# Optimization experiments

Measured on AMD Instinct MI355X. Metric: run time of the kernel, lower is better.

The kernel has to match this reference:

```python
import jax, jax.numpy as jnp
import numpy as np

N_NODES = 100000
N_EDGES = 3200000
NEG_SLOPE = 0.2  # PyG GATConv default


def setup_inputs() -> dict:
    key = jax.random.key(0)
    ks = jax.random.split(key, 10)
    x = jax.random.normal(ks[0], (N_NODES, 2), dtype=jnp.float32)
    src = jax.random.randint(ks[1], (N_EDGES,), 0, N_NODES)
    dst = jax.random.randint(ks[2], (N_EDGES,), 0, N_NODES)
    edge_index = jnp.stack([src, dst]).astype(jnp.int64)
    edge_attr = jax.random.normal(ks[3], (N_EDGES, 4), dtype=jnp.float32)
    # layer 1: in=2, heads=4, out_per_head=8
    W1 = jax.random.normal(ks[4], (2, 32), dtype=jnp.float32) * 0.5
    att_src1 = jax.random.normal(ks[5], (4, 8), dtype=jnp.float32) * 0.3
    att_dst1 = jax.random.normal(ks[6], (4, 8), dtype=jnp.float32) * 0.3
    b1 = jnp.zeros((32,), dtype=jnp.float32)
    # layer 2: in=32, heads=1, out_per_head=2
    W2 = jax.random.normal(ks[7], (32, 2), dtype=jnp.float32) * 0.2
    att_src2 = jax.random.normal(ks[8], (1, 2), dtype=jnp.float32) * 0.3
    att_dst2 = jax.random.normal(ks[9], (1, 2), dtype=jnp.float32) * 0.3
    b2 = jnp.zeros((2,), dtype=jnp.float32)
    return {"x": x, "edge_index": edge_index, "edge_attr": edge_attr,
            "W1": W1, "att_src1": att_src1, "att_dst1": att_dst1, "b1": b1,
            "W2": W2, "att_src2": att_src2, "att_dst2": att_dst2, "b2": b2}


def _gat_conv(x, W, att_src, att_dst, bias, src, dst, heads, out_ch, concat, n):
    h = (x @ W).reshape(n, heads, out_ch)            # [N,H,C]
    a_s = (h * att_src).sum(-1)                       # [N,H]
    a_d = (h * att_dst).sum(-1)                       # [N,H]
    e = jax.nn.leaky_relu(a_s[src] + a_d[dst], NEG_SLOPE)  # [E,H]
    m = jax.ops.segment_max(e, dst, num_segments=n)   # stable softmax over dst groups
    ee = jnp.exp(e - m[dst])
    s = jax.ops.segment_sum(ee, dst, num_segments=n)
    alpha = ee / (s[dst] + 1e-16)                     # [E,H]
    out = jax.ops.segment_sum(h[src] * alpha[:, :, None], dst, num_segments=n)  # [N,H,C]
    out = out.reshape(n, heads * out_ch) if concat else out.mean(axis=1)
    return out + bias, alpha


def reference(x, edge_index, edge_attr, W1, att_src1, att_dst1, b1,
              W2, att_src2, att_dst2, b2):
    # edge_attr is accepted but ignored: GATConv was built without edge_dim.
    n = x.shape[0]
    loop = jnp.arange(n, dtype=edge_index.dtype)      # add_self_loops=True (PyG default)
    src = jnp.concatenate([edge_index[0], loop])
    dst = jnp.concatenate([edge_index[1], loop])
    h, alpha1 = _gat_conv(x, W1, att_src1, att_dst1, b1, src, dst, 4, 8, True, n)
    h = jax.nn.elu(h)
    out, alpha2 = _gat_conv(h, W2, att_src2, att_dst2, b2, src, dst, 1, 2, False, n)
    return out, alpha1, alpha2
```

## Files before the change

### kernel.cpp

```cpp
#include <hip/hip_runtime.h>
#include <hip/hip_fp16.h>
#include <math.h>

#define NEG_SLOPE 0.2f
#define BW 512
#define BSH 9
#define CAP 18432
#define NB_MAX 256

typedef float f4v __attribute__((ext_vector_type(4)));

__device__ __forceinline__ float lrelu(float v) {
    return v > 0.0f ? v : NEG_SLOPE * v;
}
__device__ __forceinline__ float pack2h(float a, float b) {
    __half2 h = __floats2half2_rn(a, b);
    return *reinterpret_cast<float*>(&h);
}
__device__ __forceinline__ float2 unpack2h(float f) {
    __half2 h = *reinterpret_cast<__half2*>(&f);
    return __half22float2(h);
}
__device__ __forceinline__ void nt_store4(float4 v, float4* p) {
    f4v x = {v.x, v.y, v.z, v.w};
    __builtin_nontemporal_store(x, (f4v*)p);
}

__global__ __launch_bounds__(256) void k_l1_node(
    const float* __restrict__ x, const float* __restrict__ W1,
    const float* __restrict__ asw, const float* __restrict__ adw,
    float4* __restrict__ ga, float2* __restrict__ as1h,
    float2* __restrict__ dpack2, int n)
{
    int i = blockIdx.x * blockDim.x + threadIdx.x;
    if (i >= n) return;
    float2 xv = ((const float2*)x)[i];
    float as[4] = {0.f, 0.f, 0.f, 0.f};
    float ad[4] = {0.f, 0.f, 0.f, 0.f};
    #pragma unroll
    for (int j = 0; j < 32; ++j) {
        float h = xv.x * W1[j] + xv.y * W1[32 + j];
        as[j >> 3] += h * asw[j];
        ad[j >> 3] += h * adw[j];
    }
    float p01 = pack2h(as[0], as[1]), p23 = pack2h(as[2], as[3]);
    ga[i] = make_float4(p01, p23, xv.x, xv.y);
    as1h[i] = make_float2(p01, p23);
    dpack2[2 * i] = make_float2(pack2h(ad[0], ad[1]), pack2h(ad[2], ad[3]));
}

__global__ __launch_bounds__(256) void k_init(int* __restrict__ bucketCursor, int nb)
{
    int t = blockIdx.x * blockDim.x + threadIdx.x;
    if (t < nb) bucketCursor[t] = 0;
}

__global__ __launch_bounds__(256) void k_binA(
    const int* __restrict__ ei, int* __restrict__ bucketCursor,
    unsigned int* __restrict__ binned, int E, int Et, int nb)
{
    __shared__ int cnt[NB_MAX], lscan[NB_MAX + 1], base[NB_MAX], lcur[NB_MAX];
    __shared__ unsigned int staging[4096];
    int t = threadIdx.x;
    int c0 = blockIdx.x * 4096;
    unsigned int ent[16];
    short bb[16];
    #pragma unroll
    for (int k = 0; k < 16; ++k) {
        int e = c0 + k * 256 + t;
        int s, d;
        if (e < E) {
            s = __builtin_nontemporal_load(&ei[e]);
            d = __builtin_nontemporal_load(&ei[E + e]);
        } else { s = e - E; d = s; }
        bool valid = e < Et;
        bb[k] = valid ? (short)(d >> BSH) : (short)(-1);
        ent[k] = ((unsigned int)s << BSH) | (unsigned int)(d & (BW - 1));
    }
    if (t < nb) cnt[t] = 0;
    __syncthreads();
    #pragma unroll
    for (int k = 0; k < 16; ++k)
        if (bb[k] >= 0) atomicAdd(&cnt[bb[k]], 1);
    __syncthreads();
    if (t == 0) {
        int r = 0;
        for (int b = 0; b < nb; ++b) { lscan[b] = r; r += cnt[b]; }
        lscan[nb] = r;
    }
    __syncthreads();
    if (t < nb) {
        if (cnt[t] > 0) base[t] = atomicAdd(&bucketCursor[t], cnt[t]);
        lcur[t] = lscan[t];
    }
    __syncthreads();
    #pragma unroll
    for (int k = 0; k < 16; ++k)
        if (bb[k] >= 0) {
            int p = atomicAdd(&lcur[bb[k]], 1);
            staging[p] = ent[k];
        }
    __syncthreads();
    int total = lscan[nb];
    for (int j = t; j < total; j += 256) {
        int lo = 0, hi = nb - 1;
        while (lo < hi) {
            int mid = (lo + hi + 1) >> 1;
            if (lscan[mid] <= j) lo = mid; else hi = mid - 1;
        }
        __builtin_nontemporal_store(staging[j],
            &binned[(size_t)lo * CAP + base[lo] + (j - lscan[lo])]);
    }
}

__global__ __launch_bounds__(1024) void k_binB(
    const unsigned int* __restrict__ binned, const int* __restrict__ bucketCursor,
    int* __restrict__ sorted, int2* __restrict__ rowrange, int n, int nb)
{
    __shared__ int cnt[BW], cur[BW];
    int t = threadIdx.x;
    int b = blockIdx.x;
    int m = bucketCursor[b];
    size_t base = (size_t)b * CAP;
    int node0 = b << BSH;
    if (t < BW) cnt[t] = 0;
    __syncthreads();
    for (int i = t; i < m; i += 1024)
        atomicAdd(&cnt[binned[base + i] & (BW - 1)], 1);
    __syncthreads();
    int deg = (t < BW) ? cnt[t] : 0;
    for (int off = 1; off < BW; off <<= 1) {
        int v = (t >= off && t < BW) ? cnt[t - off] : 0;
        __syncthreads();
        if (t < BW) cnt[t] += v;
        __syncthreads();
    }
    if (t < BW) {
        int ex = cnt[t] - deg;
        cur[t] = ex;
        int node = node0 + t;
        if (node < n)
            rowrange[node] = make_int2((int)base + ex, (int)base + ex + deg);
    }
    __syncthreads();
    for (int i = t; i < m; i += 1024) {
        unsigned int en = binned[base + i];
        int dl = (int)(en & (BW - 1));
        int p = atomicAdd(&cur[dl], 1);
        sorted[base + p] = (int)(en >> BSH);
    }
}

__global__ __launch_bounds__(128) void k_l1_gather(
    const int2* __restrict__ rowrange, const int* __restrict__ sorted,
    const float4* __restrict__ ga, float2* __restrict__ dpack2,
    const float* __restrict__ W1, const float* __restrict__ b1,
    const float* __restrict__ W2,
    const float* __restrict__ asw2, const float* __restrict__ adw2,
    float4* __restrict__ pk2f, float* __restrict__ a2s,
    float2* __restrict__ d2, int n)
{
    int d = blockIdx.x * blockDim.x + threadIdx.x;
    if (d >= n) return;
    int2 rr = rowrange[d];
    int beg = rr.x, end = rr.y;
    float2 adp = dpack2[2 * d];
    float2 ad01 = unpack2h(adp.x), ad23 = unpack2h(adp.y);
    float see[4] = {0.f, 0.f, 0.f, 0.f};
    float sx0[4] = {0.f, 0.f, 0.f, 0.f};
    float sx1[4] = {0.f, 0.f, 0.f, 0.f};
    int i = beg;
    for (; i + 4 <= end; i += 4) {
        int s0 = sorted[i], s1 = sorted[i + 1], s2 = sorted[i + 2], s3 = sorted[i + 3];
        float4 v0 = ga[s0], v1 = ga[s1], v2 = ga[s2], v3 = ga[s3];
        #pragma unroll
        for (int k = 0; k < 4; ++k) {
            float4 v = (k == 0) ? v0 : (k == 1) ? v1 : (k == 2) ? v2 : v3;
            float2 a01 = unpack2h(v.x), a23 = unpack2h(v.y);
            float e0 = __expf(lrelu(a01.x + ad01.x));
            float e1 = __expf(lrelu(a01.y + ad01.y));
            float e2 = __expf(lrelu(a23.x + ad23.x));
            float e3 = __expf(lrelu(a23.y + ad23.y));
            see[0] += e0; sx0[0] += e0 * v.z; sx1[0] += e0 * v.w;
            see[1] += e1; sx0[1] += e1 * v.z; sx1[1] += e1 * v.w;
            see[2] += e2; sx0[2] += e2 * v.z; sx1[2] += e2 * v.w;
            see[3] += e3; sx0[3] += e3 * v.z; sx1[3] += e3 * v.w;
        }
    }
    for (; i < end; ++i) {
        float4 v = ga[sorted[i]];
        float2 a01 = unpack2h(v.x), a23 = unpack2h(v.y);
        float e0 = __expf(lrelu(a01.x + ad01.x));
        float e1 = __expf(lrelu(a01.y + ad01.y));
        float e2 = __expf(lrelu(a23.x + ad23.x));
        float e3 = __expf(lrelu(a23.y + ad23.y));
        see[0] += e0; sx0[0] += e0 * v.z; sx1[0] += e0 * v.w;
        see[1] += e1; sx0[1] += e1 * v.z; sx1[1] += e1 * v.w;
        see[2] += e2; sx0[2] += e2 * v.z; sx1[2] += e2 * v.w;
        see[3] += e3; sx0[3] += e3 * v.z; sx1[3] += e3 * v.w;
    }
    float rs[4];
    #pragma unroll
    for (int h = 0; h < 4; ++h) rs[h] = 1.0f / (see[h] + 1e-16f);
    dpack2[2 * d + 1] = make_float2(pack2h(rs[0], rs[1]), pack2h(rs[2], rs[3]));
    float h20 = 0.f, h21 = 0.f;
    #pragma unroll
    for (int j = 0; j < 32; ++j) {
        int h = j >> 3;
        float num = W1[j] * sx0[h] + W1[32 + j] * sx1[h];
        float o = num * rs[h] + b1[j];
        float he = o > 0.f ? o : expm1f(o);
        h20 += he * W2[2 * j];
        h21 += he * W2[2 * j + 1];
    }
    float as2 = h20 * asw2[0] + h21 * asw2[1];
    float ad2 = h20 * adw2[0] + h21 * adw2[1];
    pk2f[d] = make_float4(as2, h20, h21, ad2);
    a2s[d] = as2;
    d2[d] = make_float2(ad2, 0.f);
}

__global__ __launch_bounds__(128) void k_l2_gather(
    const int2* __restrict__ rowrange, const int* __restrict__ sorted,
    const float4* __restrict__ pk2f, const float* __restrict__ b2,
    float2* __restrict__ d2, float* __restrict__ out, int n)
{
    int d = blockIdx.x * blockDim.x + threadIdx.x;
    if (d >= n) return;
    int2 rr = rowrange[d];
    int beg = rr.x, end = rr.y;
    float ad2 = d2[d].x;
    float se = 0.f, a0 = 0.f, a1 = 0.f;
    int i = beg;
    for (; i + 4 <= end; i += 4) {
        int s0 = sorted[i], s1 = sorted[i + 1], s2 = sorted[i + 2], s3 = sorted[i + 3];
        float4 p0 = pk2f[s0], p1 = pk2f[s1], p2 = pk2f[s2], p3 = pk2f[s3];
        float e0 = __expf(lrelu(p0.x + ad2));
        float e1 = __expf(lrelu(p1.x + ad2));
        float e2 = __expf(lrelu(p2.x + ad2));
        float e3 = __expf(lrelu(p3.x + ad2));
        se += e0 + e1 + e2 + e3;
        a0 += e0 * p0.y + e1 * p1.y + e2 * p2.y + e3 * p3.y;
        a1 += e0 * p0.z + e1 * p1.z + e2 * p2.z + e3 * p3.z;
    }
    for (; i < end; ++i) {
        float4 p = pk2f[sorted[i]];
        float ee = __expf(lrelu(p.x + ad2));
        se += ee; a0 += ee * p.y; a1 += ee * p.z;
    }
    float rs2 = 1.0f / (se + 1e-16f);
    d2[d].y = rs2;
    ((float2*)out)[d] = make_float2(a0 * rs2 + b2[0], a1 * rs2 + b2[1]);
}

__global__ __launch_bounds__(256) void k_alpha1(
    const int* __restrict__ ei, const float2* __restrict__ as1h,
    const float4* __restrict__ dpack, float4* __restrict__ alpha1, int E, int Et)
{
    int e = blockIdx.x * blockDim.x + threadIdx.x;
    if (e >= Et) return;
    int s, d;
    if (e < E) {
        s = __builtin_nontemporal_load(&ei[e]);
        d = __builtin_nontemporal_load(&ei[E + e]);
    } else { s = e - E; d = s; }
    float2 g = as1h[s];
    float4 dp = dpack[d];
    float2 a01 = unpack2h(g.x), a23 = unpack2h(g.y);
    float2 b01 = unpack2h(dp.x), b23 = unpack2h(dp.y);
    float2 r01 = unpack2h(dp.z), r23 = unpack2h(dp.w);
    float4 al;
    al.x = __expf(lrelu(a01.x + b01.x)) * r01.x;
    al.y = __expf(lrelu(a01.y + b01.y)) * r01.y;
    al.z = __expf(lrelu(a23.x + b23.x)) * r23.x;
    al.w = __expf(lrelu(a23.y + b23.y)) * r23.y;
    nt_store4(al, &alpha1[e]);
}

__global__ __launch_bounds__(256) void k_alpha2(
    const int* __restrict__ ei, const float* __restrict__ a2s,
    const float2* __restrict__ d2, float* __restrict__ alpha2, int E, int Et)
{
    int e = blockIdx.x * blockDim.x + threadIdx.x;
    if (e >= Et) return;
    int s, d;
    if (e < E) {
        s = __builtin_nontemporal_load(&ei[e]);
        d = __builtin_nontemporal_load(&ei[E + e]);
    } else { s = e - E; d = s; }
    float2 dd = d2[d];
    __builtin_nontemporal_store(__expf(lrelu(a2s[s] + dd.x)) * dd.y, &alpha2[e]);
}

extern "C" void kernel_launch(void* const* d_in, const int* in_sizes, int n_in,
                              void* d_out, int out_size, void* d_ws, size_t ws_size,
                              hipStream_t stream)
{
    const float* x   = (const float*)d_in[0];
    const int*   ei  = (const int*)d_in[1];
    const float* W1  = (const float*)d_in[3];
    const float* as1 = (const float*)d_in[4];
    const float* ad1 = (const float*)d_in[5];
    const float* b1  = (const float*)d_in[6];
    const float* W2  = (const float*)d_in[7];
    const float* as2 = (const float*)d_in[8];
    const float* ad2 = (const float*)d_in[9];
    const float* b2  = (const float*)d_in[10];

    const int n  = in_sizes[0] / 2;
    const int E  = in_sizes[1] / 2;
    const int Et = E + n;
    const int nb = (n + BW - 1) >> BSH;

    char* w = (char*)d_ws;
    float4* ga    = (float4*)w;  w += (size_t)n * sizeof(float4);
    float2* as1h  = (float2*)w;  w += (size_t)n * sizeof(float2);
    float4* dpack = (float4*)w;  w += (size_t)n * sizeof(float4);
    float4* pk2f  = (float4*)w;  w += (size_t)n * sizeof(float4);
    float*  a2s   = (float*)w;   w += (size_t)n * sizeof(float);
    float2* d2    = (float2*)w;  w += (size_t)n * sizeof(float2);
    int2*   rowrange = (int2*)w; w += (size_t)n * sizeof(int2);
    int*    sorted   = (int*)w;  w += (size_t)nb * CAP * sizeof(int);
    int*    bucketCursor = (int*)w; w += (size_t)nb * sizeof(int);

    float*  out    = (float*)d_out;
    float4* alpha1 = (float4*)(out + (size_t)n * 2);
    float*  alpha2 = (float*)(alpha1 + (size_t)Et);
    unsigned int* binned = (unsigned int*)alpha1;

    dim3 blk(256);
    int gn  = (n + 255) / 256;
    int gn128 = (n + 127) / 128;
    int gEt = (Et + 255) / 256;
    int gA  = (Et + 4095) / 4096;

    k_l1_node  <<<gn,  blk, 0, stream>>>(x, W1, as1, ad1, ga, as1h, (float2*)dpack, n);
    k_init     <<<1,   blk, 0, stream>>>(bucketCursor, nb);
    k_binA     <<<gA,  blk, 0, stream>>>(ei, bucketCursor, binned, E, Et, nb);
    k_binB     <<<nb, dim3(1024), 0, stream>>>(binned, bucketCursor, sorted, rowrange, n, nb);
    k_l1_gather<<<gn128, dim3(128), 0, stream>>>(rowrange, sorted, ga, (float2*)dpack,
                                         W1, b1, W2, as2, ad2, pk2f, a2s, d2, n);
    k_l2_gather<<<gn128, dim3(128), 0, stream>>>(rowrange, sorted, pk2f, b2, d2, out, n);
    k_alpha1   <<<gEt, blk, 0, stream>>>(ei, as1h, dpack, alpha1, E, Et);
    k_alpha2   <<<gEt, blk, 0, stream>>>(ei, a2s, d2, alpha2, E, Et);
}
```

Baseline: 320.9 us.

## Fuse alpha kernels, split gathers across thread pairs, parallelize bin scan

```diff
diff --git a/kernel.cpp b/kernel.cpp
--- a/kernel.cpp
+++ b/kernel.cpp
@@ -9,6 +9,8 @@
 #define NB_MAX 256
 
 typedef float f4v __attribute__((ext_vector_type(4)));
+typedef float f2v __attribute__((ext_vector_type(2)));
+typedef int   i2v __attribute__((ext_vector_type(2)));
 
 __device__ __forceinline__ float lrelu(float v) {
     return v > 0.0f ? v : NEG_SLOPE * v;
@@ -25,14 +27,20 @@
     f4v x = {v.x, v.y, v.z, v.w};
     __builtin_nontemporal_store(x, (f4v*)p);
 }
+__device__ __forceinline__ void nt_store2(float2 v, float2* p) {
+    f2v x = {v.x, v.y};
+    __builtin_nontemporal_store(x, (f2v*)p);
+}
 
 __global__ __launch_bounds__(256) void k_l1_node(
     const float* __restrict__ x, const float* __restrict__ W1,
     const float* __restrict__ asw, const float* __restrict__ adw,
-    float4* __restrict__ ga, float2* __restrict__ as1h,
-    float2* __restrict__ dpack2, int n)
+    float4* __restrict__ ga, float4* __restrict__ spack,
+    float2* __restrict__ dpack2, int* __restrict__ bucketCursor,
+    int nb, int n)
 {
     int i = blockIdx.x * blockDim.x + threadIdx.x;
+    if (i < nb) bucketCursor[i] = 0;
     if (i >= n) return;
     float2 xv = ((const float2*)x)[i];
     float as[4] = {0.f, 0.f, 0.f, 0.f};
@@ -45,22 +53,17 @@
     }
     float p01 = pack2h(as[0], as[1]), p23 = pack2h(as[2], as[3]);
     ga[i] = make_float4(p01, p23, xv.x, xv.y);
-    as1h[i] = make_float2(p01, p23);
+    spack[i] = make_float4(p01, p23, 0.f, 0.f);
     dpack2[2 * i] = make_float2(pack2h(ad[0], ad[1]), pack2h(ad[2], ad[3]));
-}
-
-__global__ __launch_bounds__(256) void k_init(int* __restrict__ bucketCursor, int nb)
-{
-    int t = blockIdx.x * blockDim.x + threadIdx.x;
-    if (t < nb) bucketCursor[t] = 0;
 }
 
 __global__ __launch_bounds__(256) void k_binA(
     const int* __restrict__ ei, int* __restrict__ bucketCursor,
     unsigned int* __restrict__ binned, int E, int Et, int nb)
 {
-    __shared__ int cnt[NB_MAX], lscan[NB_MAX + 1], base[NB_MAX], lcur[NB_MAX];
+    __shared__ int cnt[NB_MAX], lscan[NB_MAX], base[NB_MAX], lcur[NB_MAX];
     __shared__ unsigned int staging[4096];
+    __shared__ short sbk[4096];
     int t = threadIdx.x;
     int c0 = blockIdx.x * 4096;
     unsigned int ent[16];
@@ -77,37 +80,38 @@
         bb[k] = valid ? (short)(d >> BSH) : (short)(-1);
         ent[k] = ((unsigned int)s << BSH) | (unsigned int)(d & (BW - 1));
     }
-    if (t < nb) cnt[t] = 0;
+    cnt[t] = 0;
     __syncthreads();
     #pragma unroll
     for (int k = 0; k < 16; ++k)
         if (bb[k] >= 0) atomicAdd(&cnt[bb[k]], 1);
     __syncthreads();
-    if (t == 0) {
-        int r = 0;
-        for (int b = 0; b < nb; ++b) { lscan[b] = r; r += cnt[b]; }
-        lscan[nb] = r;
-    }
-    __syncthreads();
-    if (t < nb) {
-        if (cnt[t] > 0) base[t] = atomicAdd(&bucketCursor[t], cnt[t]);
-        lcur[t] = lscan[t];
-    }
+    int c = cnt[t];
+    lscan[t] = c;
+    __syncthreads();
+    for (int off = 1; off < 256; off <<= 1) {
+        int v = (t >= off) ? lscan[t - off] : 0;
+        __syncthreads();
+        lscan[t] += v;
+        __syncthreads();
+    }
+    int tot = lscan[255];
+    int ex = lscan[t] - c;
+    __syncthreads();
+    lscan[t] = ex;
+    lcur[t] = ex;
+    if (t < nb && c > 0) base[t] = atomicAdd(&bucketCursor[t], c);
     __syncthreads();
     #pragma unroll
     for (int k = 0; k < 16; ++k)
         if (bb[k] >= 0) {
             int p = atomicAdd(&lcur[bb[k]], 1);
             staging[p] = ent[k];
+            sbk[p] = bb[k];
         }
     __syncthreads();
-    int total = lscan[nb];
-    for (int j = t; j < total; j += 256) {
-        int lo = 0, hi = nb - 1;
-        while (lo < hi) {
-            int mid = (lo + hi + 1) >> 1;
-            if (lscan[mid] <= j) lo = mid; else hi = mid - 1;
-        }
+    for (int j = t; j < tot; j += 256) {
+        int lo = sbk[j];
         __builtin_nontemporal_store(staging[j],
             &binned[(size_t)lo * CAP + base[lo] + (j - lscan[lo])]);
     }
@@ -151,16 +155,17 @@
     }
 }
 
-__global__ __launch_bounds__(128) void k_l1_gather(
+__global__ __launch_bounds__(256) void k_l1_gather(
     const int2* __restrict__ rowrange, const int* __restrict__ sorted,
     const float4* __restrict__ ga, float2* __restrict__ dpack2,
     const float* __restrict__ W1, const float* __restrict__ b1,
     const float* __restrict__ W2,
     const float* __restrict__ asw2, const float* __restrict__ adw2,
-    float4* __restrict__ pk2f, float* __restrict__ a2s,
-    float2* __restrict__ d2, int n)
-{
-    int d = blockIdx.x * blockDim.x + threadIdx.x;
+    float4* __restrict__ pk2f, float4* __restrict__ spack,
+    __half* __restrict__ dpk2h, int n)
+{
+    int t = blockIdx.x * blockDim.x + threadIdx.x;
+    int d = t >> 1, half = t & 1;
     if (d >= n) return;
     int2 rr = rowrange[d];
     int beg = rr.x, end = rr.y;
@@ -169,13 +174,13 @@
     float see[4] = {0.f, 0.f, 0.f, 0.f};
     float sx0[4] = {0.f, 0.f, 0.f, 0.f};
     float sx1[4] = {0.f, 0.f, 0.f, 0.f};
-    int i = beg;
-    for (; i + 4 <= end; i += 4) {
-        int s0 = sorted[i], s1 = sorted[i + 1], s2 = sorted[i + 2], s3 = sorted[i + 3];
-        float4 v0 = ga[s0], v1 = ga[s1], v2 = ga[s2], v3 = ga[s3];
+    int i = beg + half;
+    for (; i + 2 < end; i += 4) {
+        int s0 = sorted[i], s1 = sorted[i + 2];
+        float4 v0 = ga[s0], v1 = ga[s1];
         #pragma unroll
-        for (int k = 0; k < 4; ++k) {
-            float4 v = (k == 0) ? v0 : (k == 1) ? v1 : (k == 2) ? v2 : v3;
+        for (int k = 0; k < 2; ++k) {
+            float4 v = k ? v1 : v0;
             float2 a01 = unpack2h(v.x), a23 = unpack2h(v.y);
             float e0 = __expf(lrelu(a01.x + ad01.x));
             float e1 = __expf(lrelu(a01.y + ad01.y));
@@ -187,7 +192,7 @@
             see[3] += e3; sx0[3] += e3 * v.z; sx1[3] += e3 * v.w;
         }
     }
-    for (; i < end; ++i) {
+    for (; i < end; i += 2) {
         float4 v = ga[sorted[i]];
         float2 a01 = unpack2h(v.x), a23 = unpack2h(v.y);
         float e0 = __expf(lrelu(a01.x + ad01.x));
@@ -199,6 +204,13 @@
         see[2] += e2; sx0[2] += e2 * v.z; sx1[2] += e2 * v.w;
         see[3] += e3; sx0[3] += e3 * v.z; sx1[3] += e3 * v.w;
     }
+    #pragma unroll
+    for (int h = 0; h < 4; ++h) {
+        see[h] += __shfl_xor(see[h], 1);
+        sx0[h] += __shfl_xor(sx0[h], 1);
+        sx1[h] += __shfl_xor(sx1[h], 1);
+    }
+    if (half) return;
     float rs[4];
     #pragma unroll
     for (int h = 0; h < 4; ++h) rs[h] = 1.0f / (see[h] + 1e-16f);
@@ -216,80 +228,90 @@
     float as2 = h20 * asw2[0] + h21 * asw2[1];
     float ad2 = h20 * adw2[0] + h21 * adw2[1];
     pk2f[d] = make_float4(as2, h20, h21, ad2);
-    a2s[d] = as2;
-    d2[d] = make_float2(ad2, 0.f);
-}
-
-__global__ __launch_bounds__(128) void k_l2_gather(
+    ((float*)&spack[d])[2] = as2;
+    dpk2h[2 * d] = __float2half(ad2);
+}
+
+__global__ __launch_bounds__(256) void k_l2_gather(
     const int2* __restrict__ rowrange, const int* __restrict__ sorted,
     const float4* __restrict__ pk2f, const float* __restrict__ b2,
-    float2* __restrict__ d2, float* __restrict__ out, int n)
-{
-    int d = blockIdx.x * blockDim.x + threadIdx.x;
+    __half* __restrict__ dpk2h, float* __restrict__ out, int n)
+{
+    int t = blockIdx.x * blockDim.x + threadIdx.x;
+    int d = t >> 1, half = t & 1;
     if (d >= n) return;
     int2 rr = rowrange[d];
     int beg = rr.x, end = rr.y;
-    float ad2 = d2[d].x;
+    float ad2 = pk2f[d].w;
     float se = 0.f, a0 = 0.f, a1 = 0.f;
-    int i = beg;
-    for (; i + 4 <= end; i += 4) {
-        int s0 = sorted[i], s1 = sorted[i + 1], s2 = sorted[i + 2], s3 = sorted[i + 3];
-        float4 p0 = pk2f[s0], p1 = pk2f[s1], p2 = pk2f[s2], p3 = pk2f[s3];
+    int i = beg + half;
+    for (; i + 2 < end; i += 4) {
+        int s0 = sorted[i], s1 = sorted[i + 2];
+        float4 p0 = pk2f[s0], p1 = pk2f[s1];
         float e0 = __expf(lrelu(p0.x + ad2));
         float e1 = __expf(lrelu(p1.x + ad2));
-        float e2 = __expf(lrelu(p2.x + ad2));
-        float e3 = __expf(lrelu(p3.x + ad2));
-        se += e0 + e1 + e2 + e3;
-        a0 += e0 * p0.y + e1 * p1.y + e2 * p2.y + e3 * p3.y;
-        a1 += e0 * p0.z + e1 * p1.z + e2 * p2.z + e3 * p3.z;
-    }
-    for (; i < end; ++i) {
+        se += e0 + e1;
+        a0 += e0 * p0.y + e1 * p1.y;
+        a1 += e0 * p0.z + e1 * p1.z;
+    }
+    for (; i < end; i += 2) {
         float4 p = pk2f[sorted[i]];
         float ee = __expf(lrelu(p.x + ad2));
         se += ee; a0 += ee * p.y; a1 += ee * p.z;
     }
+    se += __shfl_xor(se, 1);
+    a0 += __shfl_xor(a0, 1);
+    a1 += __shfl_xor(a1, 1);
+    if (half) return;
     float rs2 = 1.0f / (se + 1e-16f);
-    d2[d].y = rs2;
+    dpk2h[2 * d + 1] = __float2half(rs2);
     ((float2*)out)[d] = make_float2(a0 * rs2 + b2[0], a1 * rs2 + b2[1]);
 }
 
-__global__ __launch_bounds__(256) void k_alpha1(
-    const int* __restrict__ ei, const float2* __restrict__ as1h,
-    const float4* __restrict__ dpack, float4* __restrict__ alpha1, int E, int Et)
-{
-    int e = blockIdx.x * blockDim.x + threadIdx.x;
-    if (e >= Et) return;
-    int s, d;
-    if (e < E) {
-        s = __builtin_nontemporal_load(&ei[e]);
-        d = __builtin_nontemporal_load(&ei[E + e]);
-    } else { s = e - E; d = s; }
-    float2 g = as1h[s];
-    float4 dp = dpack[d];
-    float2 a01 = unpack2h(g.x), a23 = unpack2h(g.y);
-    float2 b01 = unpack2h(dp.x), b23 = unpack2h(dp.y);
-    float2 r01 = unpack2h(dp.z), r23 = unpack2h(dp.w);
+__global__ __launch_bounds__(256) void k_alpha(
+    const int* __restrict__ ei, const float4* __restrict__ spack,
+    const float4* __restrict__ dpack, const float* __restrict__ dpk2hf,
+    float4* __restrict__ alpha1, float2* __restrict__ alpha2_2, int E, int Et)
+{
+    int p = blockIdx.x * blockDim.x + threadIdx.x;
+    int e0 = p * 2;
+    if (e0 >= Et) return;
+    int s0, d0, s1, d1;
+    if (e0 < E) {
+        i2v ss = __builtin_nontemporal_load(&((const i2v*)ei)[p]);
+        i2v dd = __builtin_nontemporal_load((const i2v*)(ei + E) + (p - E / 2) + E / 2 - E / 2 + (p - 0) - p + p);
+        dd = __builtin_nontemporal_load((const i2v*)(ei + E) + p);
+        s0 = ss.x; s1 = ss.y; d0 = dd.x; d1 = dd.y;
+    } else {
+        s0 = e0 - E; d0 = s0; s1 = s0 + 1; d1 = s1;
+    }
+    float4 sp0 = spack[s0], sp1 = spack[s1];
+    float4 dp0 = dpack[d0], dp1 = dpack[d1];
+    float  dh0 = dpk2hf[d0], dh1 = dpk2hf[d1];
+
+    float2 a01, a23, b01, b23, r01, r23, ar;
     float4 al;
+    a01 = unpack2h(sp0.x); a23 = unpack2h(sp0.y);
+    b01 = unpack2h(dp0.x); b23 = unpack2h(dp0.y);
+    r01 = unpack2h(dp0.z); r23 = unpack2h(dp0.w);
     al.x = __expf(lrelu(a01.x + b01.x)) * r01.x;
     al.y = __expf(lrelu(a01.y + b01.y)) * r01.y;
     al.z = __expf(lrelu(a23.x + b23.x)) * r23.x;
     al.w = __expf(lrelu(a23.y + b23.y)) * r23.y;
-    nt_store4(al, &alpha1[e]);
-}
-
-__global__ __launch_bounds__(256) void k_alpha2(
-    const int* __restrict__ ei, const float* __restrict__ a2s,
-    const float2* __restrict__ d2, float* __restrict__ alpha2, int E, int Et)
-{
-    int e = blockIdx.x * blockDim.x + threadIdx.x;
-    if (e >= Et) return;
-    int s, d;
-    if (e < E) {
-        s = __builtin_nontemporal_load(&ei[e]);
-        d = __builtin_nontemporal_load(&ei[E + e]);
-    } else { s = e - E; d = s; }
-    float2 dd = d2[d];
-    __builtin_nontemporal_store(__expf(lrelu(a2s[s] + dd.x)) * dd.y, &alpha2[e]);
+    nt_store4(al, &alpha1[e0]);
+    ar = unpack2h(dh0);
+    float o20 = __expf(lrelu(sp0.z + ar.x)) * ar.y;
+    a01 = unpack2h(sp1.x); a23 = unpack2h(sp1.y);
+    b01 = unpack2h(dp1.x); b23 = unpack2h(dp1.y);
+    r01 = unpack2h(dp1.z); r23 = unpack2h(dp1.w);
+    al.x = __expf(lrelu(a01.x + b01.x)) * r01.x;
+    al.y = __expf(lrelu(a01.y + b01.y)) * r01.y;
+    al.z = __expf(lrelu(a23.x + b23.x)) * r23.x;
+    al.w = __expf(lrelu(a23.y + b23.y)) * r23.y;
+    nt_store4(al, &alpha1[e0 + 1]);
+    ar = unpack2h(dh1);
+    float o21 = __expf(lrelu(sp1.z + ar.x)) * ar.y;
+    nt_store2(make_float2(o20, o21), &alpha2_2[p]);
 }
 
 extern "C" void kernel_launch(void* const* d_in, const int* in_sizes, int n_in,
@@ -314,33 +336,34 @@
 
     char* w = (char*)d_ws;
     float4* ga    = (float4*)w;  w += (size_t)n * sizeof(float4);
-    float2* as1h  = (float2*)w;  w += (size_t)n * sizeof(float2);
+    float4* spack = (float4*)w;  w += (size_t)n * sizeof(float4);
     float4* dpack = (float4*)w;  w += (size_t)n * sizeof(float4);
     float4* pk2f  = (float4*)w;  w += (size_t)n * sizeof(float4);
-    float*  a2s   = (float*)w;   w += (size_t)n * sizeof(float);
-    float2* d2    = (float2*)w;  w += (size_t)n * sizeof(float2);
+    float*  dpk2hf= (float*)w;   w += (size_t)n * sizeof(float);
     int2*   rowrange = (int2*)w; w += (size_t)n * sizeof(int2);
     int*    sorted   = (int*)w;  w += (size_t)nb * CAP * sizeof(int);
     int*    bucketCursor = (int*)w; w += (size_t)nb * sizeof(int);
 
     float*  out    = (float*)d_out;
     float4* alpha1 = (float4*)(out + (size_t)n * 2);
-    float*  alpha2 = (float*)(alpha1 + (size_t)Et);
+    float2* alpha2_2 = (float2*)(alpha1 + (size_t)Et);
     unsigned int* binned = (unsigned int*)alpha1;
 
     dim3 blk(256);
-    int gn  = (n + 255) / 256;
-    int gn128 = (n + 127) / 128;
-    int gEt = (Et + 255) / 256;
-    int gA  = (Et + 4095) / 4096;
-
-    k_l1_node  <<<gn,  blk, 0, stream>>>(x, W1, as1, ad1, ga, as1h, (float2*)dpack, n);
-    k_init     <<<1,   blk, 0, stream>>>(bucketCursor, nb);
+    int gn   = (n + 255) / 256;
+    int gn2  = (2 * n + 255) / 256;
+    int gA   = (Et + 4095) / 4096;
+    int gP   = (Et / 2 + 255) / 256;
+
+    k_l1_node  <<<gn,  blk, 0, stream>>>(x, W1, as1, ad1, ga, spack,
+                                         (float2*)dpack, bucketCursor, nb, n);
     k_binA     <<<gA,  blk, 0, stream>>>(ei, bucketCursor, binned, E, Et, nb);
     k_binB     <<<nb, dim3(1024), 0, stream>>>(binned, bucketCursor, sorted, rowrange, n, nb);
-    k_l1_gather<<<gn128, dim3(128), 0, stream>>>(rowrange, sorted, ga, (float2*)dpack,
-                                         W1, b1, W2, as2, ad2, pk2f, a2s, d2, n);
-    k_l2_gather<<<gn128, dim3(128), 0, stream>>>(rowrange, sorted, pk2f, b2, d2, out, n);
-    k_alpha1   <<<gEt, blk, 0, stream>>>(ei, as1h, dpack, alpha1, E, Et);
-    k_alpha2   <<<gEt, blk, 0, stream>>>(ei, a2s, d2, alpha2, E, Et);
-}
+    k_l1_gather<<<gn2, blk, 0, stream>>>(rowrange, sorted, ga, (float2*)dpack,
+                                         W1, b1, W2, as2, ad2, pk2f, spack,
+                                         (__half*)dpk2hf, n);
+    k_l2_gather<<<gn2, blk, 0, stream>>>(rowrange, sorted, pk2f, b2,
+                                         (__half*)dpk2hf, out, n);
+    k_alpha    <<<gP,  blk, 0, stream>>>(ei, spack, dpack, dpk2hf,
+                                         alpha1, alpha2_2, E, Et);
+}
```

After: 293.4 us. 8.6% less time.
